# Optimization experiments

Measured on AMD Instinct MI355X. Metric: run time of the kernel, lower is better.

Reference implementation:

```python
import jax, jax.numpy as jnp
import numpy as np

MARGIN = 0.3


def _pairwise_dist(x):
    # Exact euclidean cdist; same math as torch.cdist's non-mm mode:
    # sqrt(sum_k (x_i[k]-x_j[k])^2) == sqrt(|x_i|^2 + |x_j|^2 - 2 x_i.x_j).
    sq = jnp.sum(x * x, axis=1)
    sqd = sq[:, None] + sq[None, :] - 2.0 * (x @ x.T)
    sqd = jnp.maximum(sqd, 0.0)
    # safe sqrt: zero distance (diagonal) -> dist 0 with zero grad, like torch
    safe = jnp.where(sqd > 0, sqd, 1.0)
    return jnp.where(sqd > 0, jnp.sqrt(safe), 0.0)


def setup_inputs() -> dict:
    key = jax.random.key(0)
    k1, k2 = jax.random.split(key)
    n, d, n_classes = 8192, 128, 64
    inputs = jax.random.normal(k1, (n, d), dtype=jnp.float32)
    targets = jax.random.randint(k2, (n,), 0, n_classes)
    return {"inputs": inputs, "targets": targets}


def reference(inputs, targets):
    dist = _pairwise_dist(inputs)  # (n, n)
    mask = targets[:, None] == targets[None, :]  # (n, n) same-label mask
    # hard positive: max distance among same-label (diag included, as in torch code)
    dist_ap = jnp.max(jnp.where(mask, dist, -jnp.inf), axis=1)  # (n,)
    # hard negative: min distance among different-label
    dist_an = jnp.min(jnp.where(mask, jnp.inf, dist), axis=1)  # (n,)
    # MarginRankingLoss with y=1: mean(relu(-(dist_an - dist_ap) + margin))
    loss = jnp.mean(jax.nn.relu(dist_ap - dist_an + MARGIN))
    return (loss, dist)
```

## Files before the change

kernel.cpp:

```cpp
#include <hip/hip_runtime.h>
#include <hip/hip_bf16.h>
#include <cstdint>
#include <cstddef>


#define NROWS 8192
#define DIMK  128
#define MARGIN 0.3f

typedef __bf16 bf16x8 __attribute__((ext_vector_type(8)));
typedef float  f32x4  __attribute__((ext_vector_type(4)));
typedef float  f32x2  __attribute__((ext_vector_type(2)));
typedef int    i32x4  __attribute__((ext_vector_type(4)));

__device__ __forceinline__ unsigned short f2bf(float f) {
    unsigned u = __float_as_uint(f);
    u += 0x7fffu + ((u >> 16) & 1u);
    return (unsigned short)(u >> 16);
}

__global__ __launch_bounds__(256) void prep_kernel(
    const float* __restrict__ X, unsigned short* __restrict__ Xb,
    float* __restrict__ sq, int* __restrict__ ap, int* __restrict__ an)
{
    const int t = blockIdx.x * 256 + threadIdx.x;
    if (t < NROWS) { ap[t] = 0; an[t] = 0x7f800000; }
    const int row  = t >> 6;
    const int lane = t & 63;
    const f32x2 v = *(const f32x2*)(X + (size_t)row * DIMK + lane * 2);
    const unsigned short b0 = f2bf(v[0]);
    const unsigned short b1 = f2bf(v[1]);
    const int swz = (row & 7) << 4;
    *(unsigned*)((char*)Xb + (size_t)row * 256 + ((lane * 4) ^ swz)) =
        (unsigned)b0 | ((unsigned)b1 << 16);
    const float f0 = __uint_as_float((unsigned)b0 << 16);
    const float f1 = __uint_as_float((unsigned)b1 << 16);
    float s = f0 * f0 + f1 * f1;
    #pragma unroll
    for (int off = 32; off; off >>= 1) s += __shfl_xor(s, off);
    if (lane == 0) sq[row] = s;
}

__device__ __forceinline__ void store_row_shifted(float* drow, f32x4 d4, int rc) {
    const float prev = __shfl_up(d4[3], 1);
    if (rc == 0) {
        drow[0] = d4[0];
        *(f32x2*)(drow + 1) = (f32x2){d4[1], d4[2]};
    } else {
        *(f32x4*)(drow + (rc << 2) - 1) = (f32x4){prev, d4[0], d4[1], d4[2]};
    }
    if (rc == 31)
        drow[127] = d4[3];
}

__global__ __launch_bounds__(256, 2) void dist_kernel(
    const unsigned short* __restrict__ Xb, const float* __restrict__ sq,
    const int* __restrict__ tgt, float* __restrict__ dist,
    int* __restrict__ ap, int* __restrict__ an)
{
    __shared__ __align__(16) char lds[64 * 1024];
    __shared__ int apL[128], anL[128];

    const int t  = threadIdx.x;
    const int bm = blockIdx.x, bn = blockIdx.y;

    if (t < 128) { apL[t] = 0; anL[t] = 0x7f800000; }

    {
        const char* gA = (const char*)Xb + (size_t)bm * 32768;
        const char* gB = (const char*)Xb + (size_t)bn * 32768;
        #pragma unroll
        for (int i = 0; i < 8; i++) {
            const int off = i * 4096 + t * 16;
            __builtin_amdgcn_global_load_lds(
                (const __attribute__((address_space(1))) void*)(gA + off),
                (__attribute__((address_space(3))) void*)(lds + off),
                16, 0, 0);
            __builtin_amdgcn_global_load_lds(
                (const __attribute__((address_space(1))) void*)(gB + off),
                (__attribute__((address_space(3))) void*)(lds + 32768 + off),
                16, 0, 0);
        }
    }
    __syncthreads();

    const int lane = t & 63, wave = t >> 6;
    const int wm = (wave >> 1) << 6;
    const int wn = (wave & 1) << 6;
    const int l15 = lane & 15, quad = lane >> 4;
    const int rbase = bm << 7, cbase = bn << 7;
    const float INF = __int_as_float(0x7f800000);

    f32x4 acc[4][4];
    #pragma unroll
    for (int mi = 0; mi < 4; mi++)
        #pragma unroll
        for (int ni = 0; ni < 4; ni++)
            acc[mi][ni] = (f32x4){0.f, 0.f, 0.f, 0.f};

    #pragma unroll
    for (int ks = 0; ks < 4; ks++) {
        const int kb2 = ks * 64 + quad * 16;
        bf16x8 af[4], bfr[4];
        #pragma unroll
        for (int mi = 0; mi < 4; mi++) {
            const int r = wm + mi * 16 + l15;
            af[mi] = *(const bf16x8*)(lds + r * 256 + (kb2 ^ ((r & 7) << 4)));
        }
        #pragma unroll
        for (int ni = 0; ni < 4; ni++) {
            const int c = wn + ni * 16 + l15;
            bfr[ni] = *(const bf16x8*)(lds + 32768 + c * 256 + (kb2 ^ ((c & 7) << 4)));
        }
        #pragma unroll
        for (int mi = 0; mi < 4; mi++)
            #pragma unroll
            for (int ni = 0; ni < 4; ni++)
                acc[mi][ni] = __builtin_amdgcn_mfma_f32_16x16x32_bf16(
                    af[mi], bfr[ni], acc[mi][ni], 0, 0, 0);
    }

    __syncthreads();

    int lcv[4]; float sqc[4];
    #pragma unroll
    for (int ni = 0; ni < 4; ni++) {
        lcv[ni] = wn + ni * 16 + l15;
        sqc[ni] = sq[cbase + lcv[ni]];
    }
    #pragma unroll
    for (int mi = 0; mi < 4; mi++) {
        const int rl0 = wm + mi * 16 + quad * 4;
        const f32x4 sqr = *(const f32x4*)(sq + rbase + rl0);
        #pragma unroll
        for (int reg = 0; reg < 4; reg++) {
            const int rl  = rl0 + reg;
            const int rg  = rbase + rl;
            const int swz = (rl & 7) << 4;
            #pragma unroll
            for (int ni = 0; ni < 4; ni++) {
                const float sqd = sqr[reg] + sqc[ni] - 2.0f * acc[mi][ni][reg];
                float d = sqd > 0.0f ? sqrtf(sqd) : 0.0f;
                if (rg == cbase + lcv[ni]) d = 0.0f;
                *(float*)(lds + rl * 512 + ((lcv[ni] << 2) ^ swz)) = d;
            }
        }
    }
    __syncthreads();

    const int rc = t & 31;
    const int w  = t >> 5;
    float apv[4] = {-1.f, -1.f, -1.f, -1.f};
    float anv[4] = {INF, INF, INF, INF};
    const i32x4 tc = *(const i32x4*)(tgt + cbase + rc * 4);

    #pragma unroll 4
    for (int it = 0; it < 16; it++) {
        const int r = it * 8 + w;
        const f32x4 d4 = *(const f32x4*)(lds + r * 512 + ((rc ^ (r & 7)) << 4));
        const int rg = rbase + r;
        store_row_shifted(dist + (size_t)rg * NROWS + cbase, d4, rc);
        const int trg = tgt[rg];
        #pragma unroll
        for (int j = 0; j < 4; j++) {
            const bool same = (trg == tc[j]);
            apv[j] = fmaxf(apv[j], same ? d4[j] : -1.f);
            anv[j] = fminf(anv[j], same ? INF : d4[j]);
        }
    }
    #pragma unroll
    for (int j = 0; j < 4; j++) {
        apv[j] = fmaxf(apv[j], __shfl_xor(apv[j], 32));
        anv[j] = fminf(anv[j], __shfl_xor(anv[j], 32));
    }
    if (lane < 32) {
        #pragma unroll
        for (int j = 0; j < 4; j++) {
            atomicMax(apL + rc * 4 + j, __float_as_int(apv[j]));
            atomicMin(anL + rc * 4 + j, __float_as_int(anv[j]));
        }
    }
    __syncthreads();
    if (t < 128) {
        atomicMax(ap + cbase + t, apL[t]);
        atomicMin(an + cbase + t, anL[t]);
    }
}

__global__ __launch_bounds__(256) void loss_kernel(
    const int* __restrict__ ap, const int* __restrict__ an,
    float* __restrict__ out)
{
    __shared__ float red[4];
    float s = 0.0f;
    for (int i = threadIdx.x; i < NROWS; i += 256) {
        const float v = __int_as_float(ap[i]) - __int_as_float(an[i]) + MARGIN;
        s += v > 0.0f ? v : 0.0f;
    }
    #pragma unroll
    for (int off = 32; off; off >>= 1) s += __shfl_xor(s, off);
    if ((threadIdx.x & 63) == 0) red[threadIdx.x >> 6] = s;
    __syncthreads();
    if (threadIdx.x == 0)
        out[0] = (red[0] + red[1] + red[2] + red[3]) * (1.0f / NROWS);
}

extern "C" void kernel_launch(void* const* d_in, const int* in_sizes, int n_in,
                              void* d_out, int out_size, void* d_ws, size_t ws_size,
                              hipStream_t stream)
{
    const float* X   = (const float*)d_in[0];
    const int*   tgt = (const int*)d_in[1];
    float*       out = (float*)d_out;

    unsigned short* Xb = (unsigned short*)d_ws;
    float* sq = (float*)((char*)d_ws + (size_t)NROWS * DIMK * 2);
    int*   ap = (int*)(sq + NROWS);
    int*   an = ap + NROWS;

    prep_kernel<<<(NROWS * 64) / 256, 256, 0, stream>>>(X, Xb, sq, ap, an);

    dim3 grid(64, 64);
    dist_kernel<<<grid, 256, 0, stream>>>(Xb, sq, tgt, out + 1, ap, an);

    loss_kernel<<<1, 256, 0, stream>>>(ap, an, out);
}
```

Measured before the change: 332.5 us.

## Load MFMA operands directly from global and halve LDS staging for occupancy

Removes the global_load_lds staging of the A/B tiles; each lane now reads its bf16x8 fragments straight from global memory (unswizzled layout) and the LDS tile shrinks to 32KB. The epilogue transposes the 128x128 distance tile through LDS in two 64-row halves, and launch bounds are raised to 4 blocks per CU. The grid mapping is swapped so adjacent blocks share the same row panel. This trades LDS-mediated operand reuse for higher occupancy, at the cost of redundant, strided global/L2 reads and extra barriers.

```diff
diff --git a/kernel.cpp b/kernel.cpp
--- a/kernel.cpp
+++ b/kernel.cpp
@@ -30,8 +30,7 @@
     const f32x2 v = *(const f32x2*)(X + (size_t)row * DIMK + lane * 2);
     const unsigned short b0 = f2bf(v[0]);
     const unsigned short b1 = f2bf(v[1]);
-    const int swz = (row & 7) << 4;
-    *(unsigned*)((char*)Xb + (size_t)row * 256 + ((lane * 4) ^ swz)) =
+    *(unsigned*)(Xb + (size_t)row * DIMK + lane * 2) =
         (unsigned)b0 | ((unsigned)b1 << 16);
     const float f0 = __uint_as_float((unsigned)b0 << 16);
     const float f1 = __uint_as_float((unsigned)b1 << 16);
@@ -53,36 +52,18 @@
         drow[127] = d4[3];
 }
 
-__global__ __launch_bounds__(256, 2) void dist_kernel(
+__global__ __launch_bounds__(256, 4) void dist_kernel(
     const unsigned short* __restrict__ Xb, const float* __restrict__ sq,
     const int* __restrict__ tgt, float* __restrict__ dist,
     int* __restrict__ ap, int* __restrict__ an)
 {
-    __shared__ __align__(16) char lds[64 * 1024];
+    __shared__ __align__(16) char lds[32 * 1024];
     __shared__ int apL[128], anL[128];
 
     const int t  = threadIdx.x;
-    const int bm = blockIdx.x, bn = blockIdx.y;
+    const int bn = blockIdx.x, bm = blockIdx.y;
 
     if (t < 128) { apL[t] = 0; anL[t] = 0x7f800000; }
-
-    {
-        const char* gA = (const char*)Xb + (size_t)bm * 32768;
-        const char* gB = (const char*)Xb + (size_t)bn * 32768;
-        #pragma unroll
-        for (int i = 0; i < 8; i++) {
-            const int off = i * 4096 + t * 16;
-            __builtin_amdgcn_global_load_lds(
-                (const __attribute__((address_space(1))) void*)(gA + off),
-                (__attribute__((address_space(3))) void*)(lds + off),
-                16, 0, 0);
-            __builtin_amdgcn_global_load_lds(
-                (const __attribute__((address_space(1))) void*)(gB + off),
-                (__attribute__((address_space(3))) void*)(lds + 32768 + off),
-                16, 0, 0);
-        }
-    }
-    __syncthreads();
 
     const int lane = t & 63, wave = t >> 6;
     const int wm = (wave >> 1) << 6;
@@ -98,20 +79,18 @@
         for (int ni = 0; ni < 4; ni++)
             acc[mi][ni] = (f32x4){0.f, 0.f, 0.f, 0.f};
 
+    const unsigned short* Arow = Xb + (size_t)(rbase + wm + l15) * DIMK;
+    const unsigned short* Brow = Xb + (size_t)(cbase + wn + l15) * DIMK;
     #pragma unroll
     for (int ks = 0; ks < 4; ks++) {
-        const int kb2 = ks * 64 + quad * 16;
+        const int kb = ks * 32 + quad * 8;
         bf16x8 af[4], bfr[4];
         #pragma unroll
-        for (int mi = 0; mi < 4; mi++) {
-            const int r = wm + mi * 16 + l15;
-            af[mi] = *(const bf16x8*)(lds + r * 256 + (kb2 ^ ((r & 7) << 4)));
-        }
-        #pragma unroll
-        for (int ni = 0; ni < 4; ni++) {
-            const int c = wn + ni * 16 + l15;
-            bfr[ni] = *(const bf16x8*)(lds + 32768 + c * 256 + (kb2 ^ ((c & 7) << 4)));
-        }
+        for (int mi = 0; mi < 4; mi++)
+            af[mi] = *(const bf16x8*)(Arow + mi * 16 * DIMK + kb);
+        #pragma unroll
+        for (int ni = 0; ni < 4; ni++)
+            bfr[ni] = *(const bf16x8*)(Brow + ni * 16 * DIMK + kb);
         #pragma unroll
         for (int mi = 0; mi < 4; mi++)
             #pragma unroll
@@ -120,8 +99,6 @@
                     af[mi], bfr[ni], acc[mi][ni], 0, 0, 0);
     }
 
-    __syncthreads();
-
     int lcv[4]; float sqc[4];
     #pragma unroll
     for (int ni = 0; ni < 4; ni++) {
@@ -134,19 +111,17 @@
         const f32x4 sqr = *(const f32x4*)(sq + rbase + rl0);
         #pragma unroll
         for (int reg = 0; reg < 4; reg++) {
-            const int rl  = rl0 + reg;
-            const int rg  = rbase + rl;
-            const int swz = (rl & 7) << 4;
+            const int rl = rl0 + reg;
+            const int rg = rbase + rl;
             #pragma unroll
             for (int ni = 0; ni < 4; ni++) {
                 const float sqd = sqr[reg] + sqc[ni] - 2.0f * acc[mi][ni][reg];
                 float d = sqd > 0.0f ? sqrtf(sqd) : 0.0f;
                 if (rg == cbase + lcv[ni]) d = 0.0f;
-                *(float*)(lds + rl * 512 + ((lcv[ni] << 2) ^ swz)) = d;
+                acc[mi][ni][reg] = d;
             }
         }
     }
-    __syncthreads();
 
     const int rc = t & 31;
     const int w  = t >> 5;
@@ -154,20 +129,41 @@
     float anv[4] = {INF, INF, INF, INF};
     const i32x4 tc = *(const i32x4*)(tgt + cbase + rc * 4);
 
-    #pragma unroll 4
-    for (int it = 0; it < 16; it++) {
-        const int r = it * 8 + w;
-        const f32x4 d4 = *(const f32x4*)(lds + r * 512 + ((rc ^ (r & 7)) << 4));
-        const int rg = rbase + r;
-        store_row_shifted(dist + (size_t)rg * NROWS + cbase, d4, rc);
-        const int trg = tgt[rg];
-        #pragma unroll
-        for (int j = 0; j < 4; j++) {
-            const bool same = (trg == tc[j]);
-            apv[j] = fmaxf(apv[j], same ? d4[j] : -1.f);
-            anv[j] = fminf(anv[j], same ? INF : d4[j]);
-        }
-    }
+    #pragma unroll
+    for (int h = 0; h < 2; h++) {
+        if (wm == h * 64) {
+            #pragma unroll
+            for (int mi = 0; mi < 4; mi++) {
+                #pragma unroll
+                for (int reg = 0; reg < 4; reg++) {
+                    const int rl = mi * 16 + quad * 4 + reg;
+                    const int sw = (rl & 7) << 4;
+                    #pragma unroll
+                    for (int ni = 0; ni < 4; ni++)
+                        *(float*)(lds + rl * 512 + ((lcv[ni] << 2) ^ sw)) =
+                            acc[mi][ni][reg];
+                }
+            }
+        }
+        __syncthreads();
+        #pragma unroll
+        for (int it = 0; it < 8; it++) {
+            const int r = it * 8 + w;
+            const f32x4 d4 = *(const f32x4*)(
+                lds + r * 512 + (((rc) << 4) ^ ((r & 7) << 4)));
+            const int rowg = rbase + h * 64 + r;
+            store_row_shifted(dist + (size_t)rowg * NROWS + cbase, d4, rc);
+            const int trg = tgt[rowg];
+            #pragma unroll
+            for (int j = 0; j < 4; j++) {
+                const bool same = (trg == tc[j]);
+                apv[j] = fmaxf(apv[j], same ? d4[j] : -1.f);
+                anv[j] = fminf(anv[j], same ? INF : d4[j]);
+            }
+        }
+        __syncthreads();
+    }
+
     #pragma unroll
     for (int j = 0; j < 4; j++) {
         apv[j] = fmaxf(apv[j], __shfl_xor(apv[j], 32));
```

Measured after the change: 452.0 us. +35.9%, slower.
